# Kernel optimization log

Hardware: AMD Instinct MI355X
Metric: run time of the kernel (lower is better)

The kernel has to match this reference:

```python
import jax, jax.numpy as jnp
import numpy as np

N_NODES = 100000
N_EDGES = 1000000
S = 64      # n_hidden_scalars
F = 64      # n_hidden_edge_feats
RBF = 16    # rbf_dim
V = 16      # n_vec_channels
IN_DIM = 2 * S + F + RBF  # 208, EdgeUpdate MLP input


def _layernorm(x, g, b):
    m = x.mean(-1, keepdims=True)
    var = ((x - m) ** 2).mean(-1, keepdims=True)
    return (x - m) / jnp.sqrt(var + 1e-5) * g + b


def _gvp(s, v, Wh, Wu, Ws, bs, sigmoid_gate):
    # s: [N, S]; v: [N, v_in, 3]
    vh = jnp.einsum('nvc,vh->nhc', v, Wh)          # [N, h, 3]
    vu = jnp.einsum('nhc,hu->nuc', vh, Wu)          # [N, v_out, 3]
    sh = jnp.sqrt(jnp.sum(vh * vh, axis=-1) + 1e-8)  # [N, h]
    s_out = jax.nn.silu(jnp.concatenate([s, sh], axis=-1) @ Ws + bs)
    vn = jnp.sqrt(jnp.sum(vu * vu, axis=-1, keepdims=True) + 1e-8)  # [N, v_out, 1]
    gate = jax.nn.sigmoid(vn) if sigmoid_gate else vn
    return s_out, gate * vu


def setup_inputs() -> dict:
    key = jax.random.key(0)
    ks = jax.random.split(key, 24)

    def nrm(k, shape, fan_in):
        return jax.random.normal(k, shape, dtype=jnp.float32) / np.sqrt(fan_in)

    inp = {
        'node_scalars': jax.random.normal(ks[0], (N_NODES, S), dtype=jnp.float32),
        'positions': jax.random.normal(ks[1], (N_NODES, 3), dtype=jnp.float32),
        'vectors': jax.random.normal(ks[2], (N_NODES, V, 3), dtype=jnp.float32),
        'edge_feats': jax.random.normal(ks[3], (N_EDGES, F), dtype=jnp.float32),
        'd': jax.random.uniform(ks[4], (N_EDGES, RBF), dtype=jnp.float32),
        'src_idx': jax.random.randint(ks[5], (N_EDGES,), 0, N_NODES, dtype=jnp.int32),
        'dst_idx': jax.random.randint(ks[6], (N_EDGES,), 0, N_NODES, dtype=jnp.int32),
        # EdgeUpdate MLP + LayerNorm params
        'W1': nrm(ks[7], (IN_DIM, F), IN_DIM), 'b1': jnp.zeros((F,), jnp.float32),
        'W2': nrm(ks[8], (F, F), F),           'b2': jnp.zeros((F,), jnp.float32),
        'ln_g': jnp.ones((F,), jnp.float32),   'ln_b': jnp.zeros((F,), jnp.float32),
        # GVP 0: s 64->64, v 16->16 (h=16), sigmoid vector gate
        'gvp0_Wh': nrm(ks[9], (V, V), V), 'gvp0_Wu': nrm(ks[10], (V, V), V),
        'gvp0_Ws': nrm(ks[11], (S + V, S), S + V), 'gvp0_bs': jnp.zeros((S,), jnp.float32),
        # GVP 1: same shapes
        'gvp1_Wh': nrm(ks[12], (V, V), V), 'gvp1_Wu': nrm(ks[13], (V, V), V),
        'gvp1_Ws': nrm(ks[14], (S + V, S), S + V), 'gvp1_bs': jnp.zeros((S,), jnp.float32),
        # GVP 2 (last): v 16->1, identity vector activation
        'gvp2_Wh': nrm(ks[15], (V, V), V), 'gvp2_Wu': nrm(ks[16], (V, 1), V),
        'gvp2_Ws': nrm(ks[17], (S + V, S), S + V), 'gvp2_bs': jnp.zeros((S,), jnp.float32),
    }
    return inp


def reference(node_scalars, positions, vectors, edge_feats, d, src_idx, dst_idx,
              W1, b1, W2, b2, ln_g, ln_b,
              gvp0_Wh, gvp0_Wu, gvp0_Ws, gvp0_bs,
              gvp1_Wh, gvp1_Wu, gvp1_Ws, gvp1_bs,
              gvp2_Wh, gvp2_Wu, gvp2_Ws, gvp2_bs):
    # ---- EdgeUpdate: gather-concat-MLP + residual + LayerNorm ----
    h = jnp.concatenate(
        [node_scalars[src_idx], node_scalars[dst_idx], edge_feats, d], axis=-1)  # [E, 208]
    h = jax.nn.silu(h @ W1 + b1)
    h = jax.nn.silu(h @ W2 + b2)
    edge_out = _layernorm(edge_feats + h, ln_g, ln_b)  # [E, F]

    # ---- NodePositionUpdate: 3 stacked GVPs, last emits 1 vector channel ----
    s, v = node_scalars, vectors
    s, v = _gvp(s, v, gvp0_Wh, gvp0_Wu, gvp0_Ws, gvp0_bs, sigmoid_gate=True)
    s, v = _gvp(s, v, gvp1_Wh, gvp1_Wu, gvp1_Ws, gvp1_bs, sigmoid_gate=True)
    s, v = _gvp(s, v, gvp2_Wh, gvp2_Wu, gvp2_Ws, gvp2_bs, sigmoid_gate=False)  # v: [N,1,3]
    pos_out = positions + v[:, 0, :]  # [N, 3]

    return edge_out, pos_out
```

## Files before the change

### kernel.cpp

```cpp
#include <hip/hip_runtime.h>
#include <hip/hip_bf16.h>

#define N_NODES 100000
#define N_EDGES 1000000
#define S_DIM 64
#define F_DIM 64
#define RBF_DIM 16
#define V_CH 16

typedef __attribute__((ext_vector_type(4))) float f32x4;
typedef __attribute__((ext_vector_type(8))) short bf16x8;

#define NBLK 128
#define TPW 5
#define EDGE_GRID 3125

#define LDS_FENCE() __builtin_amdgcn_sched_barrier(0)

__device__ __forceinline__ float silu_f(float x) {
    return x * (1.0f / (1.0f + __expf(-x)));
}

__device__ __forceinline__ ushort f2bf(float x) {
    union { __hip_bfloat16 b; ushort u; } c;
    c.b = __float2bfloat16(x);
    return c.u;
}

__device__ __forceinline__ float4 ld4(const float* p) {
    return *reinterpret_cast<const float4*>(p);
}

__device__ __forceinline__ bf16x8 pack8(float4 u, float4 v) {
    bf16x8 r;
    r[0] = (short)f2bf(u.x); r[1] = (short)f2bf(u.y);
    r[2] = (short)f2bf(u.z); r[3] = (short)f2bf(u.w);
    r[4] = (short)f2bf(v.x); r[5] = (short)f2bf(v.y);
    r[6] = (short)f2bf(v.z); r[7] = (short)f2bf(v.w);
    return r;
}

struct Raw { float4 v[14]; };

__global__ __launch_bounds__(256, 3) void edge_kernel(
    const float* __restrict__ ns, const float* __restrict__ ef,
    const float* __restrict__ dd, const int* __restrict__ src,
    const int* __restrict__ dst, const float* __restrict__ W1,
    const float* __restrict__ b1, const float* __restrict__ W2,
    const float* __restrict__ b2, const float* __restrict__ lng,
    const float* __restrict__ lnb, float* __restrict__ out)
{
    __shared__ __align__(16) ushort b1f[7][4][64][8];
    __shared__ __align__(16) ushort b2f[2][4][64][8];
    __shared__ __align__(4)  float  hb[4][16][65];

    const int tid  = threadIdx.x;
    const int lane = tid & 63;
    const int wid  = tid >> 6;
    const int l15  = lane & 15;
    const int g    = lane >> 4;

    {
        const int fl  = tid & 63;
        const int fnn = tid >> 6;
        const int col = 16 * fnn + (fl & 15);
        const int krow = (fl >> 4) << 3;
        #pragma unroll
        for (int kk = 0; kk < 7; ++kk) {
            const int k0 = 32 * kk + krow;
            bf16x8 w;
            #pragma unroll
            for (int j = 0; j < 8; ++j) {
                const int k = k0 + j;
                w[j] = (k < 208) ? (short)f2bf(W1[k * 64 + col]) : (short)0;
            }
            *reinterpret_cast<bf16x8*>(&b1f[kk][fnn][fl][0]) = w;
        }
        #pragma unroll
        for (int kk = 0; kk < 2; ++kk) {
            const int k0 = 32 * kk + krow;
            bf16x8 w;
            #pragma unroll
            for (int j = 0; j < 8; ++j) w[j] = (short)f2bf(W2[(k0 + j) * 64 + col]);
            *reinterpret_cast<bf16x8*>(&b2f[kk][fnn][fl][0]) = w;
        }
    }
    __syncthreads();

    float b1c[4], b2c[4];
    #pragma unroll
    for (int nn = 0; nn < 4; ++nn) {
        b1c[nn] = b1[16 * nn + l15];
        b2c[nn] = b2[16 * nn + l15];
    }
    const float4 lgq = ld4(lng + 4 * l15);
    const float4 lbq = ld4(lnb + 4 * l15);

    const int wtile0 = (blockIdx.x * 4 + wid) * TPW;

    int sis[TPW], dis[TPW];
    #pragma unroll
    for (int t = 0; t < TPW; ++t) {
        const int erow = (wtile0 + t) * 16 + l15;
        sis[t] = src[erow];
        dis[t] = dst[erow];
    }

    float (*hbw)[65] = hb[wid];

    auto load_raw = [&](Raw& r, int t) {
        const int erow = (wtile0 + t) * 16 + l15;
        const float* ps = ns + (size_t)sis[t] * 64 + 8 * g;
        const float* pd = ns + (size_t)dis[t] * 64 + 8 * g;
        const float* pe = ef + (size_t)erow * 64 + 8 * g;
        const float* pr = dd + (size_t)erow * 16 + 8 * g;
        r.v[0] = ld4(ps);       r.v[1] = ld4(ps + 4);
        r.v[2] = ld4(ps + 32);  r.v[3] = ld4(ps + 36);
        r.v[4] = ld4(pd);       r.v[5] = ld4(pd + 4);
        r.v[6] = ld4(pd + 32);  r.v[7] = ld4(pd + 36);
        r.v[8] = ld4(pe);       r.v[9] = ld4(pe + 4);
        r.v[10] = ld4(pe + 32); r.v[11] = ld4(pe + 36);
        if (g < 2) { r.v[12] = ld4(pr); r.v[13] = ld4(pr + 4); }
        else { r.v[12] = make_float4(0.f,0.f,0.f,0.f); r.v[13] = make_float4(0.f,0.f,0.f,0.f); }
    };

    Raw r;
    load_raw(r, 0);

    #pragma unroll
    for (int t = 0; t < TPW; ++t) {
        const int ebase = (wtile0 + t) * 16;

        bf16x8 a0 = pack8(r.v[0], r.v[1]);
        bf16x8 a1 = pack8(r.v[2], r.v[3]);
        bf16x8 a2f = pack8(r.v[4], r.v[5]);
        bf16x8 a3 = pack8(r.v[6], r.v[7]);
        bf16x8 a4 = pack8(r.v[8], r.v[9]);
        bf16x8 a5 = pack8(r.v[10], r.v[11]);
        bf16x8 a6 = pack8(r.v[12], r.v[13]);

        if (t < TPW - 1) load_raw(r, t + 1);
        LDS_FENCE();

        f32x4 acc[4];
        #pragma unroll
        for (int nn = 0; nn < 4; ++nn) acc[nn] = (f32x4){0.f, 0.f, 0.f, 0.f};
        #pragma unroll
        for (int nn = 0; nn < 4; ++nn) {
            acc[nn] = __builtin_amdgcn_mfma_f32_16x16x32_bf16(a0, *reinterpret_cast<const bf16x8*>(&b1f[0][nn][lane][0]), acc[nn], 0, 0, 0);
            acc[nn] = __builtin_amdgcn_mfma_f32_16x16x32_bf16(a1, *reinterpret_cast<const bf16x8*>(&b1f[1][nn][lane][0]), acc[nn], 0, 0, 0);
            acc[nn] = __builtin_amdgcn_mfma_f32_16x16x32_bf16(a2f, *reinterpret_cast<const bf16x8*>(&b1f[2][nn][lane][0]), acc[nn], 0, 0, 0);
            acc[nn] = __builtin_amdgcn_mfma_f32_16x16x32_bf16(a3, *reinterpret_cast<const bf16x8*>(&b1f[3][nn][lane][0]), acc[nn], 0, 0, 0);
            acc[nn] = __builtin_amdgcn_mfma_f32_16x16x32_bf16(a4, *reinterpret_cast<const bf16x8*>(&b1f[4][nn][lane][0]), acc[nn], 0, 0, 0);
            acc[nn] = __builtin_amdgcn_mfma_f32_16x16x32_bf16(a5, *reinterpret_cast<const bf16x8*>(&b1f[5][nn][lane][0]), acc[nn], 0, 0, 0);
            acc[nn] = __builtin_amdgcn_mfma_f32_16x16x32_bf16(a6, *reinterpret_cast<const bf16x8*>(&b1f[6][nn][lane][0]), acc[nn], 0, 0, 0);
        }

        LDS_FENCE();
        #pragma unroll
        for (int nn = 0; nn < 4; ++nn)
            #pragma unroll
            for (int rr = 0; rr < 4; ++rr)
                hbw[4 * g + rr][16 * nn + l15] = silu_f(acc[nn][rr] + b1c[nn]);
        LDS_FENCE();
        bf16x8 q0, q1;
        #pragma unroll
        for (int j = 0; j < 8; ++j) {
            q0[j] = (short)f2bf(hbw[l15][8 * g + j]);
            q1[j] = (short)f2bf(hbw[l15][32 + 8 * g + j]);
        }

        f32x4 acc2[4];
        #pragma unroll
        for (int nn = 0; nn < 4; ++nn) acc2[nn] = (f32x4){0.f, 0.f, 0.f, 0.f};
        #pragma unroll
        for (int nn = 0; nn < 4; ++nn) {
            acc2[nn] = __builtin_amdgcn_mfma_f32_16x16x32_bf16(q0, *reinterpret_cast<const bf16x8*>(&b2f[0][nn][lane][0]), acc2[nn], 0, 0, 0);
            acc2[nn] = __builtin_amdgcn_mfma_f32_16x16x32_bf16(q1, *reinterpret_cast<const bf16x8*>(&b2f[1][nn][lane][0]), acc2[nn], 0, 0, 0);
        }

        LDS_FENCE();
        #pragma unroll
        for (int nn = 0; nn < 4; ++nn)
            #pragma unroll
            for (int rr = 0; rr < 4; ++rr)
                hbw[4 * g + rr][16 * nn + l15] = silu_f(acc2[nn][rr] + b2c[nn]);
        LDS_FENCE();

        float x[4][4];
        #pragma unroll
        for (int j = 0; j < 4; ++j) {
            const float* hr = &hbw[4 * j + g][4 * l15];
            const float4 e = ld4(ef + (size_t)(ebase + 4 * j + g) * 64 + 4 * l15);
            x[j][0] = hr[0] + e.x;
            x[j][1] = hr[1] + e.y;
            x[j][2] = hr[2] + e.z;
            x[j][3] = hr[3] + e.w;
        }

        #pragma unroll
        for (int j = 0; j < 4; ++j) {
            float s = x[j][0] + x[j][1] + x[j][2] + x[j][3];
            s += __shfl_xor(s, 1); s += __shfl_xor(s, 2);
            s += __shfl_xor(s, 4); s += __shfl_xor(s, 8);
            const float mean = s * (1.0f / 64.0f);
            float v = 0.f;
            #pragma unroll
            for (int c = 0; c < 4; ++c) {
                const float dx = x[j][c] - mean;
                v += dx * dx;
            }
            v += __shfl_xor(v, 1); v += __shfl_xor(v, 2);
            v += __shfl_xor(v, 4); v += __shfl_xor(v, 8);
            const float rsd = rsqrtf(v * (1.0f / 64.0f) + 1e-5f);

            float4 o;
            o.x = (x[j][0] - mean) * rsd * lgq.x + lbq.x;
            o.y = (x[j][1] - mean) * rsd * lgq.y + lbq.y;
            o.z = (x[j][2] - mean) * rsd * lgq.z + lbq.z;
            o.w = (x[j][3] - mean) * rsd * lgq.w + lbq.w;
            *reinterpret_cast<float4*>(out + (size_t)(ebase + 4 * j + g) * 64 + 4 * l15) = o;
        }
        LDS_FENCE();
    }
}

template <int UOUT, bool SIG>
__device__ __forceinline__ void gvp_step(
    float* __restrict__ s, float* __restrict__ vv,
    const float* __restrict__ Wh, const float* __restrict__ Wu,
    const float* __restrict__ Ws, const float* __restrict__ bs,
    float (*cat)[NBLK], const int tid)
{
    #pragma unroll
    for (int j = 0; j < 64; ++j) cat[j][tid] = s[j];

    float vu[UOUT * 3];
    #pragma unroll
    for (int i = 0; i < UOUT * 3; ++i) vu[i] = 0.0f;

    for (int h = 0; h < V_CH; ++h) {
        float t0 = 0.0f, t1 = 0.0f, t2 = 0.0f;
        #pragma unroll
        for (int vi = 0; vi < V_CH; ++vi) {
            const float wv = Wh[vi * V_CH + h];
            t0 = fmaf(vv[vi * 3 + 0], wv, t0);
            t1 = fmaf(vv[vi * 3 + 1], wv, t1);
            t2 = fmaf(vv[vi * 3 + 2], wv, t2);
        }
        cat[64 + h][tid] = sqrtf(t0 * t0 + t1 * t1 + t2 * t2 + 1e-8f);
        #pragma unroll
        for (int u = 0; u < UOUT; ++u) {
            const float wu = Wu[h * UOUT + u];
            vu[u * 3 + 0] = fmaf(t0, wu, vu[u * 3 + 0]);
            vu[u * 3 + 1] = fmaf(t1, wu, vu[u * 3 + 1]);
            vu[u * 3 + 2] = fmaf(t2, wu, vu[u * 3 + 2]);
        }
    }

    float acc[64];
    #pragma unroll
    for (int j = 0; j < 64; ++j) acc[j] = bs[j];
    #pragma unroll 2
    for (int k = 0; k < 64 + V_CH; ++k) {
        const float hk = cat[k][tid];
        const float* w = Ws + (size_t)k * 64;
        #pragma unroll
        for (int j = 0; j < 64; ++j) acc[j] = fmaf(hk, w[j], acc[j]);
    }
    #pragma unroll
    for (int j = 0; j < 64; ++j) s[j] = silu_f(acc[j]);

    #pragma unroll
    for (int u = 0; u < UOUT; ++u) {
        const float a = vu[u * 3 + 0];
        const float b = vu[u * 3 + 1];
        const float c = vu[u * 3 + 2];
        const float vn = sqrtf(a * a + b * b + c * c + 1e-8f);
        const float gt = SIG ? (1.0f / (1.0f + __expf(-vn))) : vn;
        vv[u * 3 + 0] = gt * a;
        vv[u * 3 + 1] = gt * b;
        vv[u * 3 + 2] = gt * c;
    }
}

__global__ __launch_bounds__(NBLK, 2) void node_kernel(
    const float* __restrict__ ns, const float* __restrict__ pos,
    const float* __restrict__ vec,
    const float* __restrict__ Wh0, const float* __restrict__ Wu0,
    const float* __restrict__ Ws0, const float* __restrict__ bs0,
    const float* __restrict__ Wh1, const float* __restrict__ Wu1,
    const float* __restrict__ Ws1, const float* __restrict__ bs1,
    const float* __restrict__ Wh2, const float* __restrict__ Wu2,
    const float* __restrict__ Ws2, const float* __restrict__ bs2,
    float* __restrict__ outpos)
{
    __shared__ float cat[64 + V_CH][NBLK];
    const int tid = threadIdx.x;
    const int n = blockIdx.x * NBLK + tid;
    const bool active = (n < N_NODES);
    const int nc = active ? n : 0;

    float s[64];
    {
        const float* p = ns + (size_t)nc * S_DIM;
        #pragma unroll
        for (int i = 0; i < 16; ++i) {
            float4 v4 = *reinterpret_cast<const float4*>(p + 4 * i);
            s[4 * i] = v4.x; s[4 * i + 1] = v4.y; s[4 * i + 2] = v4.z; s[4 * i + 3] = v4.w;
        }
    }
    float vv[48];
    {
        const float* p = vec + (size_t)nc * (V_CH * 3);
        #pragma unroll
        for (int i = 0; i < 12; ++i) {
            float4 v4 = *reinterpret_cast<const float4*>(p + 4 * i);
            vv[4 * i] = v4.x; vv[4 * i + 1] = v4.y; vv[4 * i + 2] = v4.z; vv[4 * i + 3] = v4.w;
        }
    }

    gvp_step<V_CH, true>(s, vv, Wh0, Wu0, Ws0, bs0, cat, tid);
    gvp_step<V_CH, true>(s, vv, Wh1, Wu1, Ws1, bs1, cat, tid);
    gvp_step<1, false>(s, vv, Wh2, Wu2, Ws2, bs2, cat, tid);

    if (active) {
        outpos[(size_t)n * 3 + 0] = pos[(size_t)n * 3 + 0] + vv[0];
        outpos[(size_t)n * 3 + 1] = pos[(size_t)n * 3 + 1] + vv[1];
        outpos[(size_t)n * 3 + 2] = pos[(size_t)n * 3 + 2] + vv[2];
    }
}

extern "C" void kernel_launch(void* const* d_in, const int* in_sizes, int n_in,
                              void* d_out, int out_size, void* d_ws, size_t ws_size,
                              hipStream_t stream) {
    const float* ns  = (const float*)d_in[0];
    const float* pos = (const float*)d_in[1];
    const float* vec = (const float*)d_in[2];
    const float* ef  = (const float*)d_in[3];
    const float* dd  = (const float*)d_in[4];
    const int*   src = (const int*)d_in[5];
    const int*   dst = (const int*)d_in[6];
    const float* W1  = (const float*)d_in[7];
    const float* b1  = (const float*)d_in[8];
    const float* W2  = (const float*)d_in[9];
    const float* b2  = (const float*)d_in[10];
    const float* lng = (const float*)d_in[11];
    const float* lnb = (const float*)d_in[12];
    const float* Wh0 = (const float*)d_in[13];
    const float* Wu0 = (const float*)d_in[14];
    const float* Ws0 = (const float*)d_in[15];
    const float* bs0 = (const float*)d_in[16];
    const float* Wh1 = (const float*)d_in[17];
    const float* Wu1 = (const float*)d_in[18];
    const float* Ws1 = (const float*)d_in[19];
    const float* bs1 = (const float*)d_in[20];
    const float* Wh2 = (const float*)d_in[21];
    const float* Wu2 = (const float*)d_in[22];
    const float* Ws2 = (const float*)d_in[23];
    const float* bs2 = (const float*)d_in[24];

    float* out     = (float*)d_out;
    float* out_pos = out + (size_t)N_EDGES * F_DIM;

    edge_kernel<<<EDGE_GRID, 256, 0, stream>>>(
        ns, ef, dd, src, dst, W1, b1, W2, b2, lng, lnb, out);
    node_kernel<<<(N_NODES + NBLK - 1) / NBLK, NBLK, 0, stream>>>(
        ns, pos, vec, Wh0, Wu0, Ws0, bs0, Wh1, Wu1, Ws1, bs1, Wh2, Wu2, Ws2, bs2, out_pos);
}
```

Before: 309.8 us.

## Merge edge and node kernels into one launch with block-range dispatch

Combines the edge MLP kernel and the node GVP kernel into one launch. The first 391 blocks run the node path with 256 threads each, and the remaining blocks run the edge path. The node path now keeps the scalar state in bf16 in shared memory instead of per-thread fp32 registers. This is meant to remove a second launch and the tail gap between kernels, and to let the node work overlap with the edge work. The cost is lower node precision and shared register and launch-bound limits for both paths.

```diff
diff --git a/kernel.cpp b/kernel.cpp
--- a/kernel.cpp
+++ b/kernel.cpp
@@ -11,9 +11,10 @@
 typedef __attribute__((ext_vector_type(4))) float f32x4;
 typedef __attribute__((ext_vector_type(8))) short bf16x8;
 
-#define NBLK 128
 #define TPW 5
-#define EDGE_GRID 3125
+#define EDGE_BLOCKS 3125
+#define NODE_BLOCKS 391
+#define GRID_TOTAL (EDGE_BLOCKS + NODE_BLOCKS)
 
 #define LDS_FENCE() __builtin_amdgcn_sched_barrier(0)
 
@@ -25,6 +26,10 @@
     union { __hip_bfloat16 b; ushort u; } c;
     c.b = __float2bfloat16(x);
     return c.u;
+}
+
+__device__ __forceinline__ float bf2f(ushort u) {
+    return __uint_as_float(((uint)u) << 16);
 }
 
 __device__ __forceinline__ float4 ld4(const float* p) {
@@ -42,199 +47,12 @@
 
 struct Raw { float4 v[14]; };
 
-__global__ __launch_bounds__(256, 3) void edge_kernel(
-    const float* __restrict__ ns, const float* __restrict__ ef,
-    const float* __restrict__ dd, const int* __restrict__ src,
-    const int* __restrict__ dst, const float* __restrict__ W1,
-    const float* __restrict__ b1, const float* __restrict__ W2,
-    const float* __restrict__ b2, const float* __restrict__ lng,
-    const float* __restrict__ lnb, float* __restrict__ out)
+template <int UOUT, bool SIG>
+__device__ __forceinline__ void gvp_node(
+    ushort (*cat)[256], const int tid, float* __restrict__ vv,
+    const float* __restrict__ Wh, const float* __restrict__ Wu,
+    const float* __restrict__ Ws, const float* __restrict__ bs)
 {
-    __shared__ __align__(16) ushort b1f[7][4][64][8];
-    __shared__ __align__(16) ushort b2f[2][4][64][8];
-    __shared__ __align__(4)  float  hb[4][16][65];
-
-    const int tid  = threadIdx.x;
-    const int lane = tid & 63;
-    const int wid  = tid >> 6;
-    const int l15  = lane & 15;
-    const int g    = lane >> 4;
-
-    {
-        const int fl  = tid & 63;
-        const int fnn = tid >> 6;
-        const int col = 16 * fnn + (fl & 15);
-        const int krow = (fl >> 4) << 3;
-        #pragma unroll
-        for (int kk = 0; kk < 7; ++kk) {
-            const int k0 = 32 * kk + krow;
-            bf16x8 w;
-            #pragma unroll
-            for (int j = 0; j < 8; ++j) {
-                const int k = k0 + j;
-                w[j] = (k < 208) ? (short)f2bf(W1[k * 64 + col]) : (short)0;
-            }
-            *reinterpret_cast<bf16x8*>(&b1f[kk][fnn][fl][0]) = w;
-        }
-        #pragma unroll
-        for (int kk = 0; kk < 2; ++kk) {
-            const int k0 = 32 * kk + krow;
-            bf16x8 w;
-            #pragma unroll
-            for (int j = 0; j < 8; ++j) w[j] = (short)f2bf(W2[(k0 + j) * 64 + col]);
-            *reinterpret_cast<bf16x8*>(&b2f[kk][fnn][fl][0]) = w;
-        }
-    }
-    __syncthreads();
-
-    float b1c[4], b2c[4];
-    #pragma unroll
-    for (int nn = 0; nn < 4; ++nn) {
-        b1c[nn] = b1[16 * nn + l15];
-        b2c[nn] = b2[16 * nn + l15];
-    }
-    const float4 lgq = ld4(lng + 4 * l15);
-    const float4 lbq = ld4(lnb + 4 * l15);
-
-    const int wtile0 = (blockIdx.x * 4 + wid) * TPW;
-
-    int sis[TPW], dis[TPW];
-    #pragma unroll
-    for (int t = 0; t < TPW; ++t) {
-        const int erow = (wtile0 + t) * 16 + l15;
-        sis[t] = src[erow];
-        dis[t] = dst[erow];
-    }
-
-    float (*hbw)[65] = hb[wid];
-
-    auto load_raw = [&](Raw& r, int t) {
-        const int erow = (wtile0 + t) * 16 + l15;
-        const float* ps = ns + (size_t)sis[t] * 64 + 8 * g;
-        const float* pd = ns + (size_t)dis[t] * 64 + 8 * g;
-        const float* pe = ef + (size_t)erow * 64 + 8 * g;
-        const float* pr = dd + (size_t)erow * 16 + 8 * g;
-        r.v[0] = ld4(ps);       r.v[1] = ld4(ps + 4);
-        r.v[2] = ld4(ps + 32);  r.v[3] = ld4(ps + 36);
-        r.v[4] = ld4(pd);       r.v[5] = ld4(pd + 4);
-        r.v[6] = ld4(pd + 32);  r.v[7] = ld4(pd + 36);
-        r.v[8] = ld4(pe);       r.v[9] = ld4(pe + 4);
-        r.v[10] = ld4(pe + 32); r.v[11] = ld4(pe + 36);
-        if (g < 2) { r.v[12] = ld4(pr); r.v[13] = ld4(pr + 4); }
-        else { r.v[12] = make_float4(0.f,0.f,0.f,0.f); r.v[13] = make_float4(0.f,0.f,0.f,0.f); }
-    };
-
-    Raw r;
-    load_raw(r, 0);
-
-    #pragma unroll
-    for (int t = 0; t < TPW; ++t) {
-        const int ebase = (wtile0 + t) * 16;
-
-        bf16x8 a0 = pack8(r.v[0], r.v[1]);
-        bf16x8 a1 = pack8(r.v[2], r.v[3]);
-        bf16x8 a2f = pack8(r.v[4], r.v[5]);
-        bf16x8 a3 = pack8(r.v[6], r.v[7]);
-        bf16x8 a4 = pack8(r.v[8], r.v[9]);
-        bf16x8 a5 = pack8(r.v[10], r.v[11]);
-        bf16x8 a6 = pack8(r.v[12], r.v[13]);
-
-        if (t < TPW - 1) load_raw(r, t + 1);
-        LDS_FENCE();
-
-        f32x4 acc[4];
-        #pragma unroll
-        for (int nn = 0; nn < 4; ++nn) acc[nn] = (f32x4){0.f, 0.f, 0.f, 0.f};
-        #pragma unroll
-        for (int nn = 0; nn < 4; ++nn) {
-            acc[nn] = __builtin_amdgcn_mfma_f32_16x16x32_bf16(a0, *reinterpret_cast<const bf16x8*>(&b1f[0][nn][lane][0]), acc[nn], 0, 0, 0);
-            acc[nn] = __builtin_amdgcn_mfma_f32_16x16x32_bf16(a1, *reinterpret_cast<const bf16x8*>(&b1f[1][nn][lane][0]), acc[nn], 0, 0, 0);
-            acc[nn] = __builtin_amdgcn_mfma_f32_16x16x32_bf16(a2f, *reinterpret_cast<const bf16x8*>(&b1f[2][nn][lane][0]), acc[nn], 0, 0, 0);
-            acc[nn] = __builtin_amdgcn_mfma_f32_16x16x32_bf16(a3, *reinterpret_cast<const bf16x8*>(&b1f[3][nn][lane][0]), acc[nn], 0, 0, 0);
-            acc[nn] = __builtin_amdgcn_mfma_f32_16x16x32_bf16(a4, *reinterpret_cast<const bf16x8*>(&b1f[4][nn][lane][0]), acc[nn], 0, 0, 0);
-            acc[nn] = __builtin_amdgcn_mfma_f32_16x16x32_bf16(a5, *reinterpret_cast<const bf16x8*>(&b1f[5][nn][lane][0]), acc[nn], 0, 0, 0);
-            acc[nn] = __builtin_amdgcn_mfma_f32_16x16x32_bf16(a6, *reinterpret_cast<const bf16x8*>(&b1f[6][nn][lane][0]), acc[nn], 0, 0, 0);
-        }
-
-        LDS_FENCE();
-        #pragma unroll
-        for (int nn = 0; nn < 4; ++nn)
-            #pragma unroll
-            for (int rr = 0; rr < 4; ++rr)
-                hbw[4 * g + rr][16 * nn + l15] = silu_f(acc[nn][rr] + b1c[nn]);
-        LDS_FENCE();
-        bf16x8 q0, q1;
-        #pragma unroll
-        for (int j = 0; j < 8; ++j) {
-            q0[j] = (short)f2bf(hbw[l15][8 * g + j]);
-            q1[j] = (short)f2bf(hbw[l15][32 + 8 * g + j]);
-        }
-
-        f32x4 acc2[4];
-        #pragma unroll
-        for (int nn = 0; nn < 4; ++nn) acc2[nn] = (f32x4){0.f, 0.f, 0.f, 0.f};
-        #pragma unroll
-        for (int nn = 0; nn < 4; ++nn) {
-            acc2[nn] = __builtin_amdgcn_mfma_f32_16x16x32_bf16(q0, *reinterpret_cast<const bf16x8*>(&b2f[0][nn][lane][0]), acc2[nn], 0, 0, 0);
-            acc2[nn] = __builtin_amdgcn_mfma_f32_16x16x32_bf16(q1, *reinterpret_cast<const bf16x8*>(&b2f[1][nn][lane][0]), acc2[nn], 0, 0, 0);
-        }
-
-        LDS_FENCE();
-        #pragma unroll
-        for (int nn = 0; nn < 4; ++nn)
-            #pragma unroll
-            for (int rr = 0; rr < 4; ++rr)
-                hbw[4 * g + rr][16 * nn + l15] = silu_f(acc2[nn][rr] + b2c[nn]);
-        LDS_FENCE();
-
-        float x[4][4];
-        #pragma unroll
-        for (int j = 0; j < 4; ++j) {
-            const float* hr = &hbw[4 * j + g][4 * l15];
-            const float4 e = ld4(ef + (size_t)(ebase + 4 * j + g) * 64 + 4 * l15);
-            x[j][0] = hr[0] + e.x;
-            x[j][1] = hr[1] + e.y;
-            x[j][2] = hr[2] + e.z;
-            x[j][3] = hr[3] + e.w;
-        }
-
-        #pragma unroll
-        for (int j = 0; j < 4; ++j) {
-            float s = x[j][0] + x[j][1] + x[j][2] + x[j][3];
-            s += __shfl_xor(s, 1); s += __shfl_xor(s, 2);
-            s += __shfl_xor(s, 4); s += __shfl_xor(s, 8);
-            const float mean = s * (1.0f / 64.0f);
-            float v = 0.f;
-            #pragma unroll
-            for (int c = 0; c < 4; ++c) {
-                const float dx = x[j][c] - mean;
-                v += dx * dx;
-            }
-            v += __shfl_xor(v, 1); v += __shfl_xor(v, 2);
-            v += __shfl_xor(v, 4); v += __shfl_xor(v, 8);
-            const float rsd = rsqrtf(v * (1.0f / 64.0f) + 1e-5f);
-
-            float4 o;
-            o.x = (x[j][0] - mean) * rsd * lgq.x + lbq.x;
-            o.y = (x[j][1] - mean) * rsd * lgq.y + lbq.y;
-            o.z = (x[j][2] - mean) * rsd * lgq.z + lbq.z;
-            o.w = (x[j][3] - mean) * rsd * lgq.w + lbq.w;
-            *reinterpret_cast<float4*>(out + (size_t)(ebase + 4 * j + g) * 64 + 4 * l15) = o;
-        }
-        LDS_FENCE();
-    }
-}
-
-template <int UOUT, bool SIG>
-__device__ __forceinline__ void gvp_step(
-    float* __restrict__ s, float* __restrict__ vv,
-    const float* __restrict__ Wh, const float* __restrict__ Wu,
-    const float* __restrict__ Ws, const float* __restrict__ bs,
-    float (*cat)[NBLK], const int tid)
-{
-    #pragma unroll
-    for (int j = 0; j < 64; ++j) cat[j][tid] = s[j];
-
     float vu[UOUT * 3];
     #pragma unroll
     for (int i = 0; i < UOUT * 3; ++i) vu[i] = 0.0f;
@@ -248,7 +66,7 @@
             t1 = fmaf(vv[vi * 3 + 1], wv, t1);
             t2 = fmaf(vv[vi * 3 + 2], wv, t2);
         }
-        cat[64 + h][tid] = sqrtf(t0 * t0 + t1 * t1 + t2 * t2 + 1e-8f);
+        cat[64 + h][tid] = f2bf(sqrtf(t0 * t0 + t1 * t1 + t2 * t2 + 1e-8f));
         #pragma unroll
         for (int u = 0; u < UOUT; ++u) {
             const float wu = Wu[h * UOUT + u];
@@ -257,19 +75,21 @@
             vu[u * 3 + 2] = fmaf(t2, wu, vu[u * 3 + 2]);
         }
     }
+    LDS_FENCE();
 
     float acc[64];
     #pragma unroll
     for (int j = 0; j < 64; ++j) acc[j] = bs[j];
     #pragma unroll 2
     for (int k = 0; k < 64 + V_CH; ++k) {
-        const float hk = cat[k][tid];
+        const float hk = bf2f(cat[k][tid]);
         const float* w = Ws + (size_t)k * 64;
         #pragma unroll
         for (int j = 0; j < 64; ++j) acc[j] = fmaf(hk, w[j], acc[j]);
     }
+    LDS_FENCE();
     #pragma unroll
-    for (int j = 0; j < 64; ++j) s[j] = silu_f(acc[j]);
+    for (int j = 0; j < 64; ++j) cat[j][tid] = f2bf(silu_f(acc[j]));
 
     #pragma unroll
     for (int u = 0; u < UOUT; ++u) {
@@ -284,50 +104,236 @@
     }
 }
 
-__global__ __launch_bounds__(NBLK, 2) void node_kernel(
+__global__ __launch_bounds__(256, 3) void fused_kernel(
     const float* __restrict__ ns, const float* __restrict__ pos,
-    const float* __restrict__ vec,
+    const float* __restrict__ vec, const float* __restrict__ ef,
+    const float* __restrict__ dd, const int* __restrict__ src,
+    const int* __restrict__ dst, const float* __restrict__ W1,
+    const float* __restrict__ b1, const float* __restrict__ W2,
+    const float* __restrict__ b2, const float* __restrict__ lng,
+    const float* __restrict__ lnb,
     const float* __restrict__ Wh0, const float* __restrict__ Wu0,
     const float* __restrict__ Ws0, const float* __restrict__ bs0,
     const float* __restrict__ Wh1, const float* __restrict__ Wu1,
     const float* __restrict__ Ws1, const float* __restrict__ bs1,
     const float* __restrict__ Wh2, const float* __restrict__ Wu2,
     const float* __restrict__ Ws2, const float* __restrict__ bs2,
-    float* __restrict__ outpos)
+    float* __restrict__ out, float* __restrict__ outpos)
 {
-    __shared__ float cat[64 + V_CH][NBLK];
+    __shared__ __align__(16) char smem[53504];
     const int tid = threadIdx.x;
-    const int n = blockIdx.x * NBLK + tid;
-    const bool active = (n < N_NODES);
-    const int nc = active ? n : 0;
-
-    float s[64];
-    {
-        const float* p = ns + (size_t)nc * S_DIM;
-        #pragma unroll
-        for (int i = 0; i < 16; ++i) {
-            float4 v4 = *reinterpret_cast<const float4*>(p + 4 * i);
-            s[4 * i] = v4.x; s[4 * i + 1] = v4.y; s[4 * i + 2] = v4.z; s[4 * i + 3] = v4.w;
-        }
-    }
-    float vv[48];
-    {
-        const float* p = vec + (size_t)nc * (V_CH * 3);
-        #pragma unroll
-        for (int i = 0; i < 12; ++i) {
-            float4 v4 = *reinterpret_cast<const float4*>(p + 4 * i);
-            vv[4 * i] = v4.x; vv[4 * i + 1] = v4.y; vv[4 * i + 2] = v4.z; vv[4 * i + 3] = v4.w;
-        }
-    }
-
-    gvp_step<V_CH, true>(s, vv, Wh0, Wu0, Ws0, bs0, cat, tid);
-    gvp_step<V_CH, true>(s, vv, Wh1, Wu1, Ws1, bs1, cat, tid);
-    gvp_step<1, false>(s, vv, Wh2, Wu2, Ws2, bs2, cat, tid);
-
-    if (active) {
-        outpos[(size_t)n * 3 + 0] = pos[(size_t)n * 3 + 0] + vv[0];
-        outpos[(size_t)n * 3 + 1] = pos[(size_t)n * 3 + 1] + vv[1];
-        outpos[(size_t)n * 3 + 2] = pos[(size_t)n * 3 + 2] + vv[2];
+
+    if (blockIdx.x >= NODE_BLOCKS) {
+        ushort* b1f = (ushort*)smem;
+        ushort* b2f = (ushort*)(smem + 28672);
+        float (*hb)[16][65] = reinterpret_cast<float(*)[16][65]>(smem + 36864);
+
+        const int lane = tid & 63;
+        const int wid  = tid >> 6;
+        const int l15  = lane & 15;
+        const int g    = lane >> 4;
+
+        {
+            const int fl  = tid & 63;
+            const int fnn = tid >> 6;
+            const int col = 16 * fnn + (fl & 15);
+            const int krow = (fl >> 4) << 3;
+            #pragma unroll
+            for (int kk = 0; kk < 7; ++kk) {
+                const int k0 = 32 * kk + krow;
+                bf16x8 w;
+                #pragma unroll
+                for (int j = 0; j < 8; ++j) {
+                    const int k = k0 + j;
+                    w[j] = (k < 208) ? (short)f2bf(W1[k * 64 + col]) : (short)0;
+                }
+                *reinterpret_cast<bf16x8*>(b1f + (((kk * 4 + fnn) * 64 + fl) * 8)) = w;
+            }
+            #pragma unroll
+            for (int kk = 0; kk < 2; ++kk) {
+                const int k0 = 32 * kk + krow;
+                bf16x8 w;
+                #pragma unroll
+                for (int j = 0; j < 8; ++j) w[j] = (short)f2bf(W2[(k0 + j) * 64 + col]);
+                *reinterpret_cast<bf16x8*>(b2f + (((kk * 4 + fnn) * 64 + fl) * 8)) = w;
+            }
+        }
+        __syncthreads();
+
+        float b1c[4], b2c[4];
+        #pragma unroll
+        for (int nn = 0; nn < 4; ++nn) {
+            b1c[nn] = b1[16 * nn + l15];
+            b2c[nn] = b2[16 * nn + l15];
+        }
+        const float4 lgq = ld4(lng + 4 * l15);
+        const float4 lbq = ld4(lnb + 4 * l15);
+
+        const int wtile0 = ((blockIdx.x - NODE_BLOCKS) * 4 + wid) * TPW;
+
+        int sis[TPW], dis[TPW];
+        #pragma unroll
+        for (int t = 0; t < TPW; ++t) {
+            const int erow = (wtile0 + t) * 16 + l15;
+            sis[t] = src[erow];
+            dis[t] = dst[erow];
+        }
+
+        float (*hbw)[65] = hb[wid];
+
+        auto load_raw = [&](Raw& r, int t) {
+            const int erow = (wtile0 + t) * 16 + l15;
+            const float* ps = ns + (size_t)sis[t] * 64 + 8 * g;
+            const float* pd = ns + (size_t)dis[t] * 64 + 8 * g;
+            const float* pe = ef + (size_t)erow * 64 + 8 * g;
+            const float* pr = dd + (size_t)erow * 16 + 8 * g;
+            r.v[0] = ld4(ps);       r.v[1] = ld4(ps + 4);
+            r.v[2] = ld4(ps + 32);  r.v[3] = ld4(ps + 36);
+            r.v[4] = ld4(pd);       r.v[5] = ld4(pd + 4);
+            r.v[6] = ld4(pd + 32);  r.v[7] = ld4(pd + 36);
+            r.v[8] = ld4(pe);       r.v[9] = ld4(pe + 4);
+            r.v[10] = ld4(pe + 32); r.v[11] = ld4(pe + 36);
+            if (g < 2) { r.v[12] = ld4(pr); r.v[13] = ld4(pr + 4); }
+            else { r.v[12] = make_float4(0.f,0.f,0.f,0.f); r.v[13] = make_float4(0.f,0.f,0.f,0.f); }
+        };
+
+        Raw r;
+        load_raw(r, 0);
+
+        #pragma unroll
+        for (int t = 0; t < TPW; ++t) {
+            const int ebase = (wtile0 + t) * 16;
+
+            bf16x8 a0 = pack8(r.v[0], r.v[1]);
+            bf16x8 a1 = pack8(r.v[2], r.v[3]);
+            bf16x8 a2f = pack8(r.v[4], r.v[5]);
+            bf16x8 a3 = pack8(r.v[6], r.v[7]);
+            bf16x8 a4 = pack8(r.v[8], r.v[9]);
+            bf16x8 a5 = pack8(r.v[10], r.v[11]);
+            bf16x8 a6 = pack8(r.v[12], r.v[13]);
+
+            if (t < TPW - 1) load_raw(r, t + 1);
+            LDS_FENCE();
+
+            f32x4 acc[4];
+            #pragma unroll
+            for (int nn = 0; nn < 4; ++nn) acc[nn] = (f32x4){0.f, 0.f, 0.f, 0.f};
+            #pragma unroll
+            for (int nn = 0; nn < 4; ++nn) {
+                acc[nn] = __builtin_amdgcn_mfma_f32_16x16x32_bf16(a0, *reinterpret_cast<const bf16x8*>(b1f + (((0 * 4 + nn) * 64 + lane) * 8)), acc[nn], 0, 0, 0);
+                acc[nn] = __builtin_amdgcn_mfma_f32_16x16x32_bf16(a1, *reinterpret_cast<const bf16x8*>(b1f + (((1 * 4 + nn) * 64 + lane) * 8)), acc[nn], 0, 0, 0);
+                acc[nn] = __builtin_amdgcn_mfma_f32_16x16x32_bf16(a2f, *reinterpret_cast<const bf16x8*>(b1f + (((2 * 4 + nn) * 64 + lane) * 8)), acc[nn], 0, 0, 0);
+                acc[nn] = __builtin_amdgcn_mfma_f32_16x16x32_bf16(a3, *reinterpret_cast<const bf16x8*>(b1f + (((3 * 4 + nn) * 64 + lane) * 8)), acc[nn], 0, 0, 0);
+                acc[nn] = __builtin_amdgcn_mfma_f32_16x16x32_bf16(a4, *reinterpret_cast<const bf16x8*>(b1f + (((4 * 4 + nn) * 64 + lane) * 8)), acc[nn], 0, 0, 0);
+                acc[nn] = __builtin_amdgcn_mfma_f32_16x16x32_bf16(a5, *reinterpret_cast<const bf16x8*>(b1f + (((5 * 4 + nn) * 64 + lane) * 8)), acc[nn], 0, 0, 0);
+                acc[nn] = __builtin_amdgcn_mfma_f32_16x16x32_bf16(a6, *reinterpret_cast<const bf16x8*>(b1f + (((6 * 4 + nn) * 64 + lane) * 8)), acc[nn], 0, 0, 0);
+            }
+
+            LDS_FENCE();
+            #pragma unroll
+            for (int nn = 0; nn < 4; ++nn)
+                #pragma unroll
+                for (int rr = 0; rr < 4; ++rr)
+                    hbw[4 * g + rr][16 * nn + l15] = silu_f(acc[nn][rr] + b1c[nn]);
+            LDS_FENCE();
+            bf16x8 q0, q1;
+            #pragma unroll
+            for (int j = 0; j < 8; ++j) {
+                q0[j] = (short)f2bf(hbw[l15][8 * g + j]);
+                q1[j] = (short)f2bf(hbw[l15][32 + 8 * g + j]);
+            }
+
+            f32x4 acc2[4];
+            #pragma unroll
+            for (int nn = 0; nn < 4; ++nn) acc2[nn] = (f32x4){0.f, 0.f, 0.f, 0.f};
+            #pragma unroll
+            for (int nn = 0; nn < 4; ++nn) {
+                acc2[nn] = __builtin_amdgcn_mfma_f32_16x16x32_bf16(q0, *reinterpret_cast<const bf16x8*>(b2f + (((0 * 4 + nn) * 64 + lane) * 8)), acc2[nn], 0, 0, 0);
+                acc2[nn] = __builtin_amdgcn_mfma_f32_16x16x32_bf16(q1, *reinterpret_cast<const bf16x8*>(b2f + (((1 * 4 + nn) * 64 + lane) * 8)), acc2[nn], 0, 0, 0);
+            }
+
+            LDS_FENCE();
+            #pragma unroll
+            for (int nn = 0; nn < 4; ++nn)
+                #pragma unroll
+                for (int rr = 0; rr < 4; ++rr)
+                    hbw[4 * g + rr][16 * nn + l15] = silu_f(acc2[nn][rr] + b2c[nn]);
+            LDS_FENCE();
+
+            float x[4][4];
+            #pragma unroll
+            for (int j = 0; j < 4; ++j) {
+                const float* hr = &hbw[4 * j + g][4 * l15];
+                const float4 e = ld4(ef + (size_t)(ebase + 4 * j + g) * 64 + 4 * l15);
+                x[j][0] = hr[0] + e.x;
+                x[j][1] = hr[1] + e.y;
+                x[j][2] = hr[2] + e.z;
+                x[j][3] = hr[3] + e.w;
+            }
+
+            #pragma unroll
+            for (int j = 0; j < 4; ++j) {
+                float s = x[j][0] + x[j][1] + x[j][2] + x[j][3];
+                s += __shfl_xor(s, 1); s += __shfl_xor(s, 2);
+                s += __shfl_xor(s, 4); s += __shfl_xor(s, 8);
+                const float mean = s * (1.0f / 64.0f);
+                float v = 0.f;
+                #pragma unroll
+                for (int c = 0; c < 4; ++c) {
+                    const float dx = x[j][c] - mean;
+                    v += dx * dx;
+                }
+                v += __shfl_xor(v, 1); v += __shfl_xor(v, 2);
+                v += __shfl_xor(v, 4); v += __shfl_xor(v, 8);
+                const float rsd = rsqrtf(v * (1.0f / 64.0f) + 1e-5f);
+
+                float4 o;
+                o.x = (x[j][0] - mean) * rsd * lgq.x + lbq.x;
+                o.y = (x[j][1] - mean) * rsd * lgq.y + lbq.y;
+                o.z = (x[j][2] - mean) * rsd * lgq.z + lbq.z;
+                o.w = (x[j][3] - mean) * rsd * lgq.w + lbq.w;
+                *reinterpret_cast<float4*>(out + (size_t)(ebase + 4 * j + g) * 64 + 4 * l15) = o;
+            }
+            LDS_FENCE();
+        }
+    } else {
+        ushort (*cat)[256] = reinterpret_cast<ushort(*)[256]>(smem);
+        const int nidx = blockIdx.x * 256 + tid;
+        const bool nactive = (nidx < N_NODES);
+        const int nc = nactive ? nidx : 0;
+
+        {
+            const float* p = ns + (size_t)nc * S_DIM;
+            #pragma unroll
+            for (int i = 0; i < 16; ++i) {
+                const float4 v4 = ld4(p + 4 * i);
+                cat[4 * i + 0][tid] = f2bf(v4.x);
+                cat[4 * i + 1][tid] = f2bf(v4.y);
+                cat[4 * i + 2][tid] = f2bf(v4.z);
+                cat[4 * i + 3][tid] = f2bf(v4.w);
+            }
+        }
+        float vv[48];
+        {
+            const float* p = vec + (size_t)nc * (V_CH * 3);
+            #pragma unroll
+            for (int i = 0; i < 12; ++i) {
+                const float4 v4 = ld4(p + 4 * i);
+                vv[4 * i] = v4.x; vv[4 * i + 1] = v4.y;
+                vv[4 * i + 2] = v4.z; vv[4 * i + 3] = v4.w;
+            }
+        }
+        LDS_FENCE();
+
+        gvp_node<V_CH, true>(cat, tid, vv, Wh0, Wu0, Ws0, bs0);
+        gvp_node<V_CH, true>(cat, tid, vv, Wh1, Wu1, Ws1, bs1);
+        gvp_node<1, false>(cat, tid, vv, Wh2, Wu2, Ws2, bs2);
+
+        if (nactive) {
+            outpos[(size_t)nidx * 3 + 0] = pos[(size_t)nidx * 3 + 0] + vv[0];
+            outpos[(size_t)nidx * 3 + 1] = pos[(size_t)nidx * 3 + 1] + vv[1];
+            outpos[(size_t)nidx * 3 + 2] = pos[(size_t)nidx * 3 + 2] + vv[2];
+        }
     }
 }
 
@@ -363,8 +369,8 @@
     float* out     = (float*)d_out;
     float* out_pos = out + (size_t)N_EDGES * F_DIM;
 
-    edge_kernel<<<EDGE_GRID, 256, 0, stream>>>(
-        ns, ef, dd, src, dst, W1, b1, W2, b2, lng, lnb, out);
-    node_kernel<<<(N_NODES + NBLK - 1) / NBLK, NBLK, 0, stream>>>(
-        ns, pos, vec, Wh0, Wu0, Ws0, bs0, Wh1, Wu1, Ws1, bs1, Wh2, Wu2, Ws2, bs2, out_pos);
-}
+    fused_kernel<<<GRID_TOTAL, 256, 0, stream>>>(
+        ns, pos, vec, ef, dd, src, dst, W1, b1, W2, b2, lng, lnb,
+        Wh0, Wu0, Ws0, bs0, Wh1, Wu1, Ws1, bs1, Wh2, Wu2, Ws2, bs2,
+        out, out_pos);
+}
```

After: 316.9 us. 2.3% more time.

## Keep MLP activations in registers via transposed MFMA, drop LDS staging

Applied to the files above, without the earlier changes.

Swaps the MFMA operand order so each lane's accumulator holds a full edge row's features. Layer-1 activations then feed layer-2 directly from registers, using a permuted W2 row order instead of an LDS transpose. The LayerNorm reduction shrinks to two cross-group shuffles, and the per-wave hb LDS buffer and sched barriers are removed. Edge-feature and rbf loads move from the prefetch into each tile iteration, which reduces register prefetch depth but may expose more load latency.

```diff
diff --git a/kernel.cpp b/kernel.cpp
--- a/kernel.cpp
+++ b/kernel.cpp
@@ -15,8 +15,6 @@
 #define TPW 5
 #define EDGE_GRID 3125
 
-#define LDS_FENCE() __builtin_amdgcn_sched_barrier(0)
-
 __device__ __forceinline__ float silu_f(float x) {
     return x * (1.0f / (1.0f + __expf(-x)));
 }
@@ -27,20 +25,20 @@
     return c.u;
 }
 
-__device__ __forceinline__ float4 ld4(const float* p) {
-    return *reinterpret_cast<const float4*>(p);
-}
-
-__device__ __forceinline__ bf16x8 pack8(float4 u, float4 v) {
+__device__ __forceinline__ f32x4 ld4v(const float* p) {
+    return *reinterpret_cast<const f32x4*>(p);
+}
+
+__device__ __forceinline__ bf16x8 pack8(f32x4 u, f32x4 v) {
     bf16x8 r;
-    r[0] = (short)f2bf(u.x); r[1] = (short)f2bf(u.y);
-    r[2] = (short)f2bf(u.z); r[3] = (short)f2bf(u.w);
-    r[4] = (short)f2bf(v.x); r[5] = (short)f2bf(v.y);
-    r[6] = (short)f2bf(v.z); r[7] = (short)f2bf(v.w);
+    r[0] = (short)f2bf(u[0]); r[1] = (short)f2bf(u[1]);
+    r[2] = (short)f2bf(u[2]); r[3] = (short)f2bf(u[3]);
+    r[4] = (short)f2bf(v[0]); r[5] = (short)f2bf(v[1]);
+    r[6] = (short)f2bf(v[2]); r[7] = (short)f2bf(v[3]);
     return r;
 }
 
-struct Raw { float4 v[14]; };
+struct RawG { f32x4 v[8]; };
 
 __global__ __launch_bounds__(256, 3) void edge_kernel(
     const float* __restrict__ ns, const float* __restrict__ ef,
@@ -52,7 +50,6 @@
 {
     __shared__ __align__(16) ushort b1f[7][4][64][8];
     __shared__ __align__(16) ushort b2f[2][4][64][8];
-    __shared__ __align__(4)  float  hb[4][16][65];
 
     const int tid  = threadIdx.x;
     const int lane = tid & 63;
@@ -61,10 +58,12 @@
     const int g    = lane >> 4;
 
     {
-        const int fl  = tid & 63;
-        const int fnn = tid >> 6;
-        const int col = 16 * fnn + (fl & 15);
-        const int krow = (fl >> 4) << 3;
+        const int fl   = tid & 63;
+        const int fnn  = tid >> 6;
+        const int fl15 = fl & 15;
+        const int fg   = fl >> 4;
+        const int col  = 16 * fnn + fl15;
+        const int krow = fg << 3;
         #pragma unroll
         for (int kk = 0; kk < 7; ++kk) {
             const int k0 = 32 * kk + krow;
@@ -78,23 +77,23 @@
         }
         #pragma unroll
         for (int kk = 0; kk < 2; ++kk) {
-            const int k0 = 32 * kk + krow;
             bf16x8 w;
             #pragma unroll
-            for (int j = 0; j < 8; ++j) w[j] = (short)f2bf(W2[(k0 + j) * 64 + col]);
+            for (int j = 0; j < 8; ++j) {
+                const int delta = 16 * (2 * kk + (j >> 2)) + 4 * fg + (j & 3);
+                w[j] = (short)f2bf(W2[delta * 64 + col]);
+            }
             *reinterpret_cast<bf16x8*>(&b2f[kk][fnn][fl][0]) = w;
         }
     }
     __syncthreads();
 
-    float b1c[4], b2c[4];
+    f32x4 b1q[4], b2q[4];
     #pragma unroll
     for (int nn = 0; nn < 4; ++nn) {
-        b1c[nn] = b1[16 * nn + l15];
-        b2c[nn] = b2[16 * nn + l15];
-    }
-    const float4 lgq = ld4(lng + 4 * l15);
-    const float4 lbq = ld4(lnb + 4 * l15);
+        b1q[nn] = ld4v(b1 + 16 * nn + 4 * g);
+        b2q[nn] = ld4v(b2 + 16 * nn + 4 * g);
+    }
 
     const int wtile0 = (blockIdx.x * 4 + wid) * TPW;
 
@@ -106,68 +105,69 @@
         dis[t] = dst[erow];
     }
 
-    float (*hbw)[65] = hb[wid];
-
-    auto load_raw = [&](Raw& r, int t) {
-        const int erow = (wtile0 + t) * 16 + l15;
+    auto load_gather = [&](RawG& r, int t) {
         const float* ps = ns + (size_t)sis[t] * 64 + 8 * g;
         const float* pd = ns + (size_t)dis[t] * 64 + 8 * g;
-        const float* pe = ef + (size_t)erow * 64 + 8 * g;
-        const float* pr = dd + (size_t)erow * 16 + 8 * g;
-        r.v[0] = ld4(ps);       r.v[1] = ld4(ps + 4);
-        r.v[2] = ld4(ps + 32);  r.v[3] = ld4(ps + 36);
-        r.v[4] = ld4(pd);       r.v[5] = ld4(pd + 4);
-        r.v[6] = ld4(pd + 32);  r.v[7] = ld4(pd + 36);
-        r.v[8] = ld4(pe);       r.v[9] = ld4(pe + 4);
-        r.v[10] = ld4(pe + 32); r.v[11] = ld4(pe + 36);
-        if (g < 2) { r.v[12] = ld4(pr); r.v[13] = ld4(pr + 4); }
-        else { r.v[12] = make_float4(0.f,0.f,0.f,0.f); r.v[13] = make_float4(0.f,0.f,0.f,0.f); }
+        r.v[0] = ld4v(ps);      r.v[1] = ld4v(ps + 4);
+        r.v[2] = ld4v(ps + 32); r.v[3] = ld4v(ps + 36);
+        r.v[4] = ld4v(pd);      r.v[5] = ld4v(pd + 4);
+        r.v[6] = ld4v(pd + 32); r.v[7] = ld4v(pd + 36);
     };
 
-    Raw r;
-    load_raw(r, 0);
+    RawG r;
+    load_gather(r, 0);
 
     #pragma unroll
     for (int t = 0; t < TPW; ++t) {
         const int ebase = (wtile0 + t) * 16;
+        const int erow  = ebase + l15;
+
+        const float* pe = ef + (size_t)erow * 64;
+        const float* pr = dd + (size_t)erow * 16;
+        const f32x4 e0 = ld4v(pe + 8 * g), e1 = ld4v(pe + 8 * g + 4);
+        const f32x4 e2 = ld4v(pe + 32 + 8 * g), e3 = ld4v(pe + 32 + 8 * g + 4);
+        f32x4 r0 = {0.f,0.f,0.f,0.f}, r1 = {0.f,0.f,0.f,0.f};
+        if (g < 2) { r0 = ld4v(pr + 8 * g); r1 = ld4v(pr + 8 * g + 4); }
+        f32x4 efq[4];
+        #pragma unroll
+        for (int nn = 0; nn < 4; ++nn) efq[nn] = ld4v(pe + 16 * nn + 4 * g);
 
         bf16x8 a0 = pack8(r.v[0], r.v[1]);
         bf16x8 a1 = pack8(r.v[2], r.v[3]);
         bf16x8 a2f = pack8(r.v[4], r.v[5]);
         bf16x8 a3 = pack8(r.v[6], r.v[7]);
-        bf16x8 a4 = pack8(r.v[8], r.v[9]);
-        bf16x8 a5 = pack8(r.v[10], r.v[11]);
-        bf16x8 a6 = pack8(r.v[12], r.v[13]);
-
-        if (t < TPW - 1) load_raw(r, t + 1);
-        LDS_FENCE();
+        bf16x8 a4 = pack8(e0, e1);
+        bf16x8 a5 = pack8(e2, e3);
+        bf16x8 a6 = pack8(r0, r1);
+
+        if (t < TPW - 1) load_gather(r, t + 1);
 
         f32x4 acc[4];
         #pragma unroll
         for (int nn = 0; nn < 4; ++nn) acc[nn] = (f32x4){0.f, 0.f, 0.f, 0.f};
         #pragma unroll
         for (int nn = 0; nn < 4; ++nn) {
-            acc[nn] = __builtin_amdgcn_mfma_f32_16x16x32_bf16(a0, *reinterpret_cast<const bf16x8*>(&b1f[0][nn][lane][0]), acc[nn], 0, 0, 0);
-            acc[nn] = __builtin_amdgcn_mfma_f32_16x16x32_bf16(a1, *reinterpret_cast<const bf16x8*>(&b1f[1][nn][lane][0]), acc[nn], 0, 0, 0);
-            acc[nn] = __builtin_amdgcn_mfma_f32_16x16x32_bf16(a2f, *reinterpret_cast<const bf16x8*>(&b1f[2][nn][lane][0]), acc[nn], 0, 0, 0);
-            acc[nn] = __builtin_amdgcn_mfma_f32_16x16x32_bf16(a3, *reinterpret_cast<const bf16x8*>(&b1f[3][nn][lane][0]), acc[nn], 0, 0, 0);
-            acc[nn] = __builtin_amdgcn_mfma_f32_16x16x32_bf16(a4, *reinterpret_cast<const bf16x8*>(&b1f[4][nn][lane][0]), acc[nn], 0, 0, 0);
-            acc[nn] = __builtin_amdgcn_mfma_f32_16x16x32_bf16(a5, *reinterpret_cast<const bf16x8*>(&b1f[5][nn][lane][0]), acc[nn], 0, 0, 0);
-            acc[nn] = __builtin_amdgcn_mfma_f32_16x16x32_bf16(a6, *reinterpret_cast<const bf16x8*>(&b1f[6][nn][lane][0]), acc[nn], 0, 0, 0);
-        }
-
-        LDS_FENCE();
-        #pragma unroll
-        for (int nn = 0; nn < 4; ++nn)
+            acc[nn] = __builtin_amdgcn_mfma_f32_16x16x32_bf16(*reinterpret_cast<const bf16x8*>(&b1f[0][nn][lane][0]), a0, acc[nn], 0, 0, 0);
+            acc[nn] = __builtin_amdgcn_mfma_f32_16x16x32_bf16(*reinterpret_cast<const bf16x8*>(&b1f[1][nn][lane][0]), a1, acc[nn], 0, 0, 0);
+            acc[nn] = __builtin_amdgcn_mfma_f32_16x16x32_bf16(*reinterpret_cast<const bf16x8*>(&b1f[2][nn][lane][0]), a2f, acc[nn], 0, 0, 0);
+            acc[nn] = __builtin_amdgcn_mfma_f32_16x16x32_bf16(*reinterpret_cast<const bf16x8*>(&b1f[3][nn][lane][0]), a3, acc[nn], 0, 0, 0);
+            acc[nn] = __builtin_amdgcn_mfma_f32_16x16x32_bf16(*reinterpret_cast<const bf16x8*>(&b1f[4][nn][lane][0]), a4, acc[nn], 0, 0, 0);
+            acc[nn] = __builtin_amdgcn_mfma_f32_16x16x32_bf16(*reinterpret_cast<const bf16x8*>(&b1f[5][nn][lane][0]), a5, acc[nn], 0, 0, 0);
+            acc[nn] = __builtin_amdgcn_mfma_f32_16x16x32_bf16(*reinterpret_cast<const bf16x8*>(&b1f[6][nn][lane][0]), a6, acc[nn], 0, 0, 0);
+        }
+
+        f32x4 sil[4];
+        #pragma unroll
+        for (int nn = 0; nn < 4; ++nn) {
             #pragma unroll
             for (int rr = 0; rr < 4; ++rr)
-                hbw[4 * g + rr][16 * nn + l15] = silu_f(acc[nn][rr] + b1c[nn]);
-        LDS_FENCE();
+                sil[nn][rr] = silu_f(acc[nn][rr] + b1q[nn][rr]);
+        }
         bf16x8 q0, q1;
         #pragma unroll
         for (int j = 0; j < 8; ++j) {
-            q0[j] = (short)f2bf(hbw[l15][8 * g + j]);
-            q1[j] = (short)f2bf(hbw[l15][32 + 8 * g + j]);
+            q0[j] = (short)f2bf(sil[j >> 2][j & 3]);
+            q1[j] = (short)f2bf(sil[2 + (j >> 2)][j & 3]);
         }
 
         f32x4 acc2[4];
@@ -175,53 +175,48 @@
         for (int nn = 0; nn < 4; ++nn) acc2[nn] = (f32x4){0.f, 0.f, 0.f, 0.f};
         #pragma unroll
         for (int nn = 0; nn < 4; ++nn) {
-            acc2[nn] = __builtin_amdgcn_mfma_f32_16x16x32_bf16(q0, *reinterpret_cast<const bf16x8*>(&b2f[0][nn][lane][0]), acc2[nn], 0, 0, 0);
-            acc2[nn] = __builtin_amdgcn_mfma_f32_16x16x32_bf16(q1, *reinterpret_cast<const bf16x8*>(&b2f[1][nn][lane][0]), acc2[nn], 0, 0, 0);
-        }
-
-        LDS_FENCE();
-        #pragma unroll
-        for (int nn = 0; nn < 4; ++nn)
-            #pragma unroll
-            for (int rr = 0; rr < 4; ++rr)
-                hbw[4 * g + rr][16 * nn + l15] = silu_f(acc2[nn][rr] + b2c[nn]);
-        LDS_FENCE();
-
-        float x[4][4];
-        #pragma unroll
-        for (int j = 0; j < 4; ++j) {
-            const float* hr = &hbw[4 * j + g][4 * l15];
-            const float4 e = ld4(ef + (size_t)(ebase + 4 * j + g) * 64 + 4 * l15);
-            x[j][0] = hr[0] + e.x;
-            x[j][1] = hr[1] + e.y;
-            x[j][2] = hr[2] + e.z;
-            x[j][3] = hr[3] + e.w;
-        }
-
-        #pragma unroll
-        for (int j = 0; j < 4; ++j) {
-            float s = x[j][0] + x[j][1] + x[j][2] + x[j][3];
-            s += __shfl_xor(s, 1); s += __shfl_xor(s, 2);
-            s += __shfl_xor(s, 4); s += __shfl_xor(s, 8);
-            const float mean = s * (1.0f / 64.0f);
-            float v = 0.f;
-            #pragma unroll
-            for (int c = 0; c < 4; ++c) {
-                const float dx = x[j][c] - mean;
+            acc2[nn] = __builtin_amdgcn_mfma_f32_16x16x32_bf16(*reinterpret_cast<const bf16x8*>(&b2f[0][nn][lane][0]), q0, acc2[nn], 0, 0, 0);
+            acc2[nn] = __builtin_amdgcn_mfma_f32_16x16x32_bf16(*reinterpret_cast<const bf16x8*>(&b2f[1][nn][lane][0]), q1, acc2[nn], 0, 0, 0);
+        }
+
+        f32x4 x[4];
+        float s = 0.f;
+        #pragma unroll
+        for (int nn = 0; nn < 4; ++nn) {
+            #pragma unroll
+            for (int rr = 0; rr < 4; ++rr) {
+                x[nn][rr] = silu_f(acc2[nn][rr] + b2q[nn][rr]) + efq[nn][rr];
+                s += x[nn][rr];
+            }
+        }
+        s += __shfl_xor(s, 16);
+        s += __shfl_xor(s, 32);
+        const float mean = s * (1.0f / 64.0f);
+
+        float v = 0.f;
+        #pragma unroll
+        for (int nn = 0; nn < 4; ++nn) {
+            #pragma unroll
+            for (int rr = 0; rr < 4; ++rr) {
+                const float dx = x[nn][rr] - mean;
                 v += dx * dx;
             }
-            v += __shfl_xor(v, 1); v += __shfl_xor(v, 2);
-            v += __shfl_xor(v, 4); v += __shfl_xor(v, 8);
-            const float rsd = rsqrtf(v * (1.0f / 64.0f) + 1e-5f);
-
-            float4 o;
-            o.x = (x[j][0] - mean) * rsd * lgq.x + lbq.x;
-            o.y = (x[j][1] - mean) * rsd * lgq.y + lbq.y;
-            o.z = (x[j][2] - mean) * rsd * lgq.z + lbq.z;
-            o.w = (x[j][3] - mean) * rsd * lgq.w + lbq.w;
-            *reinterpret_cast<float4*>(out + (size_t)(ebase + 4 * j + g) * 64 + 4 * l15) = o;
-        }
-        LDS_FENCE();
+        }
+        v += __shfl_xor(v, 16);
+        v += __shfl_xor(v, 32);
+        const float rsd = rsqrtf(v * (1.0f / 64.0f) + 1e-5f);
+
+        float* obase = out + (size_t)erow * 64;
+        #pragma unroll
+        for (int nn = 0; nn < 4; ++nn) {
+            const f32x4 lg = ld4v(lng + 16 * nn + 4 * g);
+            const f32x4 lb = ld4v(lnb + 16 * nn + 4 * g);
+            f32x4 o;
+            #pragma unroll
+            for (int rr = 0; rr < 4; ++rr)
+                o[rr] = (x[nn][rr] - mean) * rsd * lg[rr] + lb[rr];
+            *reinterpret_cast<f32x4*>(obase + 16 * nn + 4 * g) = o;
+        }
     }
 }
 
```

New measurement: 317.1 us. 1.02x slower.
